# Optimization experiments

Hardware: AMD Instinct MI355X
Metric: run time of the kernel (lower is better)

The kernel has to match this reference:

```python
import jax, jax.numpy as jnp
import numpy as np

T, B, FEAT = 256, 512, 8
HID = 256
IN_DIM = 4  # QCNN output dim


def _linear_params(key, out_dim, in_dim, scale=0.1):
    kw, kb = jax.random.split(key)
    W = jax.random.normal(kw, (out_dim, in_dim), dtype=jnp.float32) * scale
    b = jax.random.normal(kb, (out_dim,), dtype=jnp.float32) * scale
    return W, b


def setup_inputs() -> dict:
    key = jax.random.key(0)
    ks = jax.random.split(key, 12)
    inputs = jax.random.normal(ks[0], (T, B, FEAT), dtype=jnp.float32)
    # QCNN feature extractor linears (torch Linear: W is [out, in])
    fm_w, fm_b = _linear_params(ks[1], 16, FEAT)
    c1_w, c1_b = _linear_params(ks[2], 16, 16)
    p1_w, p1_b = _linear_params(ks[3], 12, 16)
    c2_w, c2_b = _linear_params(ks[4], 8, 12)
    p2_w, p2_b = _linear_params(ks[5], 4, 8)
    c3_w, c3_b = _linear_params(ks[6], 4, 4)
    # LSTM gate linears: (IN_DIM + HID) -> HID
    f_w, f_b = _linear_params(ks[7], HID, IN_DIM + HID)
    i_w, i_b = _linear_params(ks[8], HID, IN_DIM + HID)
    u_w, u_b = _linear_params(ks[9], HID, IN_DIM + HID)
    o_w, o_b = _linear_params(ks[10], HID, IN_DIM + HID)
    # tagger head: HID -> 1
    head_w, head_b = _linear_params(ks[11], 1, HID)
    return dict(inputs=inputs, fm_w=fm_w, fm_b=fm_b, c1_w=c1_w, c1_b=c1_b,
                p1_w=p1_w, p1_b=p1_b, c2_w=c2_w, c2_b=c2_b, p2_w=p2_w, p2_b=p2_b,
                c3_w=c3_w, c3_b=c3_b, f_w=f_w, f_b=f_b, i_w=i_w, i_b=i_b,
                u_w=u_w, u_b=u_b, o_w=o_w, o_b=o_b, head_w=head_w, head_b=head_b)


def _lin(x, W, b):
    return x @ W.T + b


def reference(inputs, fm_w, fm_b, c1_w, c1_b, p1_w, p1_b, c2_w, c2_b,
              p2_w, p2_b, c3_w, c3_b, f_w, f_b, i_w, i_b, u_w, u_b,
              o_w, o_b, head_w, head_b):
    seq_len, batch, _ = inputs.shape
    # QCNN feature extractor has no cross-timestep dependency -> apply to all steps at once
    x = jnp.tanh(_lin(inputs, fm_w, fm_b))
    x = jnp.tanh(_lin(x, c1_w, c1_b))
    x = jnp.tanh(_lin(x, p1_w, p1_b))
    x = jnp.tanh(_lin(x, c2_w, c2_b))
    x = jnp.tanh(_lin(x, p2_w, p2_b))
    feats = jnp.tanh(_lin(x, c3_w, c3_b))  # [T, B, 4]

    h0 = jnp.zeros((batch, HID), dtype=inputs.dtype)
    c0 = jnp.zeros((batch, HID), dtype=inputs.dtype)

    def step(carry, xt):
        hx, cx = carry
        combined = jnp.concatenate([xt, hx], axis=1)  # [B, 4+HID]
        f = jax.nn.sigmoid(_lin(combined, f_w, f_b))
        i = jax.nn.sigmoid(_lin(combined, i_w, i_b))
        g = jnp.tanh(_lin(combined, u_w, u_b))
        o = jax.nn.sigmoid(_lin(combined, o_w, o_b))
        cx = f * cx + i * g
        hx = o * jnp.tanh(cx)
        return (hx, cx), hx

    (_, _), lstm_out = jax.lax.scan(step, (h0, c0), feats)  # [T, B, HID]
    out = _lin(lstm_out, head_w, head_b)  # [T, B, 1]
    return out
```

## Files before the change

### kernel.cpp

```cpp
#include <hip/hip_runtime.h>
#include <hip/hip_bf16.h>
#include <hip/hip_fp16.h>
#include <stdint.h>

#define T_STEPS 256
#define BATCH 512

typedef _Float16 f16x8 __attribute__((ext_vector_type(8)));
typedef _Float16 h2_t  __attribute__((ext_vector_type(2)));
typedef float    f32x4 __attribute__((ext_vector_type(4)));

__device__ __forceinline__ float fdot2(uint32_t w, uint32_t c, float acc) {
#if __has_builtin(__builtin_amdgcn_fdot2)
    h2_t a, b;
    __builtin_memcpy(&a, &w, 4);
    __builtin_memcpy(&b, &c, 4);
    return __builtin_amdgcn_fdot2(a, b, acc, false);
#else
    union { uint32_t u; _Float16 h[2]; } A, B;
    A.u = w; B.u = c;
    return acc + (float)A.h[0]*(float)B.h[0] + (float)A.h[1]*(float)B.h[1];
#endif
}

__device__ __forceinline__ float sigmoidf_(float x) {
    return 1.f / (1.f + __expf(-x));
}
__device__ __forceinline__ float tanhf_(float x) {
    float ax = fabsf(x);
    float e = __expf(-2.f * ax);
    float r = (1.f - e) / (1.f + e);
    return copysignf(r, x);
}

__device__ __forceinline__ float sel4(int d, float a, float b, float c, float e) {
    float lo = (d & 1) ? b : a;
    float hi = (d & 1) ? e : c;
    return (d & 2) ? hi : lo;
}

#define MFMA_AG(c, aa, bb) \
    asm volatile("v_mfma_f32_16x16x32_f16 %0, %1, %2, %0" : "+v"(c) : "v"(aa), "a"(bb))
#define MFMA_VG(c, aa, bb) \
    asm volatile("v_mfma_f32_16x16x32_f16 %0, %1, %2, %0" : "+v"(c) : "v"(aa), "v"(bb))

__global__ void concat_qw(const float* __restrict__ fm_w, const float* __restrict__ fm_b,
                          const float* __restrict__ c1_w, const float* __restrict__ c1_b,
                          const float* __restrict__ p1_w, const float* __restrict__ p1_b,
                          const float* __restrict__ c2_w, const float* __restrict__ c2_b,
                          const float* __restrict__ p2_w, const float* __restrict__ p2_b,
                          const float* __restrict__ c3_w, const float* __restrict__ c3_b,
                          float* __restrict__ qw) {
    for (int k = threadIdx.x; k < 780; k += 256) {
        float v;
        if      (k < 128) v = fm_w[k];
        else if (k < 144) v = fm_b[k-128];
        else if (k < 400) v = c1_w[k-144];
        else if (k < 416) v = c1_b[k-400];
        else if (k < 608) v = p1_w[k-416];
        else if (k < 620) v = p1_b[k-608];
        else if (k < 716) v = c2_w[k-620];
        else if (k < 724) v = c2_b[k-716];
        else if (k < 756) v = p2_w[k-724];
        else if (k < 760) v = p2_b[k-756];
        else if (k < 776) v = c3_w[k-760];
        else              v = c3_b[k-776];
        qw[k] = v;
    }
}

__global__ void pack_bfrag(const float* __restrict__ f_w, const float* __restrict__ i_w,
                           const float* __restrict__ u_w, const float* __restrict__ o_w,
                           uint4* __restrict__ bfragsG) {
    int idx = blockIdx.x * 256 + threadIdx.x;
    int l = idx & 63, q = (idx >> 6) & 7, n = idx >> 9;
    int col = n * 16 + (l & 15);
    int g = col >> 8, j = col & 255;
    const float* W = (g == 0) ? f_w : (g == 1) ? i_w : (g == 2) ? u_w : o_w;
    union { uint4 u; _Float16 h[8]; } P;
#pragma unroll
    for (int e = 0; e < 8; ++e) {
        int k = q * 32 + ((l >> 4) * 8) + e;
        P.h[e] = (_Float16)W[j * 260 + 4 + k];
    }
    bfragsG[idx] = P.u;
}

__global__ void pack_xw(const float* __restrict__ f_w, const float* __restrict__ i_w,
                        const float* __restrict__ u_w, const float* __restrict__ o_w,
                        _Float16* __restrict__ xwG) {
    int t = blockIdx.x * 256 + threadIdx.x;
    int g = t >> 10, k = (t >> 8) & 3, j = t & 255;
    const float* W = (g == 0) ? f_w : (g == 1) ? i_w : (g == 2) ? u_w : o_w;
    xwG[t] = (_Float16)W[j * 260 + k];
}

__global__ void qcnn_kernel(const float* __restrict__ in, const float* __restrict__ qw,
                            _Float16* __restrict__ feats) {
    int r = blockIdx.x * 256 + threadIdx.x;
    const float* x = in + (size_t)r * 8;
    float v0[8];
#pragma unroll
    for (int i = 0; i < 8; ++i) v0[i] = x[i];
    float v1[16];
#pragma unroll
    for (int o = 0; o < 16; ++o) {
        float s = qw[128 + o];
#pragma unroll
        for (int i = 0; i < 8; ++i) s += qw[o*8 + i] * v0[i];
        v1[o] = tanhf_(s);
    }
    float v2[16];
#pragma unroll
    for (int o = 0; o < 16; ++o) {
        float s = qw[400 + o];
#pragma unroll
        for (int i = 0; i < 16; ++i) s += qw[144 + o*16 + i] * v1[i];
        v2[o] = tanhf_(s);
    }
    float v3[12];
#pragma unroll
    for (int o = 0; o < 12; ++o) {
        float s = qw[608 + o];
#pragma unroll
        for (int i = 0; i < 16; ++i) s += qw[416 + o*16 + i] * v2[i];
        v3[o] = tanhf_(s);
    }
    float v4[8];
#pragma unroll
    for (int o = 0; o < 8; ++o) {
        float s = qw[716 + o];
#pragma unroll
        for (int i = 0; i < 12; ++i) s += qw[620 + o*12 + i] * v3[i];
        v4[o] = tanhf_(s);
    }
    float v5[4];
#pragma unroll
    for (int o = 0; o < 4; ++o) {
        float s = qw[756 + o];
#pragma unroll
        for (int i = 0; i < 8; ++i) s += qw[724 + o*8 + i] * v4[i];
        v5[o] = tanhf_(s);
    }
    union { uint32_t u[2]; _Float16 h[4]; } P;
#pragma unroll
    for (int o = 0; o < 4; ++o) {
        float s = qw[776 + o];
#pragma unroll
        for (int i = 0; i < 4; ++i) s += qw[760 + o*4 + i] * v5[i];
        P.h[o] = (_Float16)tanhf_(s);
    }
    *reinterpret_cast<uint2*>(feats + (size_t)r * 4) = make_uint2(P.u[0], P.u[1]);
}

__global__ __launch_bounds__(256, 1)
void lstm_kernel(const uint4* __restrict__ bfragsG, const _Float16* __restrict__ xwG,
                 const _Float16* __restrict__ feats,
                 const float* __restrict__ f_b, const float* __restrict__ i_b,
                 const float* __restrict__ u_b, const float* __restrict__ o_b,
                 const float* __restrict__ head_w, const float* __restrict__ head_bp,
                 float* __restrict__ out) {
    __shared__ uint4     blds67[2][64][64];
    __shared__ __align__(16) _Float16 comb[2][2][256];
    __shared__ float     redL[2][4][2];

    const int tid = threadIdx.x;
    const int w   = tid >> 6;
    const int l   = tid & 63;
    const int d_  = l >> 4;
    const int jl  = (w * 4 + d_) * 16 + (l & 15);
    const int s0  = blockIdx.x * 2;

    for (int idx = tid; idx < 8192; idx += 256) {
        int n = idx >> 7, qq = (idx >> 6) & 1, ll = idx & 63;
        blds67[qq][n][ll] = bfragsG[(n * 8 + 6 + qq) * 64 + ll];
    }
    reinterpret_cast<uint32_t*>(&comb[0][0][0])[tid] = 0u;

    f16x8 Br03[16][4];
#pragma unroll
    for (int m = 0; m < 16; ++m) {
        const int n = (m >> 2) * 16 + w * 4 + (m & 3);
#pragma unroll
        for (int q = 0; q < 4; ++q) {
            Br03[m][q] = *reinterpret_cast<const f16x8*>(bfragsG + (n * 8 + q) * 64 + l);
            asm volatile("" : "+a"(Br03[m][q]));
        }
    }
    f16x8 Br45[16][2];
#pragma unroll
    for (int m = 0; m < 16; ++m) {
        const int n = (m >> 2) * 16 + w * 4 + (m & 3);
#pragma unroll
        for (int q = 0; q < 2; ++q) {
            Br45[m][q] = *reinterpret_cast<const f16x8*>(bfragsG + (n * 8 + 4 + q) * 64 + l);
            asm volatile("" : "+v"(Br45[m][q]));
        }
    }

    float bias_[4] = { f_b[jl], i_b[jl], u_b[jl], o_b[jl] };
    uint32_t xwp0[4], xwp1[4];
#pragma unroll
    for (int g = 0; g < 4; ++g) {
        union { uint32_t u; _Float16 h[2]; } P;
        P.h[0] = xwG[g*1024 +       jl]; P.h[1] = xwG[g*1024 + 256 + jl];
        xwp0[g] = P.u;
        P.h[0] = xwG[g*1024 + 512 + jl]; P.h[1] = xwG[g*1024 + 768 + jl];
        xwp1[g] = P.u;
    }
    const float hwj = head_w[jl];
    const float hb  = head_bp[0];
    uint2 xr0 = *reinterpret_cast<const uint2*>(feats + ((size_t)0 * BATCH + s0    ) * 4);
    uint2 xr1 = *reinterpret_cast<const uint2*>(feats + ((size_t)0 * BATCH + s0 + 1) * 4);

    __syncthreads();

    float cs0 = 0.f, cs1 = 0.f;

#pragma unroll 1
    for (int t = 0; t < T_STEPS; ++t) {
        const int cur = t & 1;
        uint2 xn0 = xr0, xn1 = xr1;
        if (t + 1 < T_STEPS) {
            xn0 = *reinterpret_cast<const uint2*>(feats + ((size_t)(t+1) * BATCH + s0    ) * 4);
            xn1 = *reinterpret_cast<const uint2*>(feats + ((size_t)(t+1) * BATCH + s0 + 1) * 4);
        }

        const _Float16* ab = &comb[cur][l & 1][(l >> 4) * 8];
        f16x8 A_[8];
#pragma unroll
        for (int q = 0; q < 8; ++q)
            A_[q] = *reinterpret_cast<const f16x8*>(ab + q * 32);

        float gv0[4], gv1[4];

#pragma unroll
        for (int g = 0; g < 4; ++g) {
            f16x8 t6[4], t7[4];
#pragma unroll
            for (int d = 0; d < 4; ++d) {
                const int n = g * 16 + w * 4 + d;
                t6[d] = *reinterpret_cast<const f16x8*>(&blds67[0][n][l]);
                t7[d] = *reinterpret_cast<const f16x8*>(&blds67[1][n][l]);
            }

            f32x4 c0 = {0.f,0.f,0.f,0.f}, c1 = {0.f,0.f,0.f,0.f};
            f32x4 c2 = {0.f,0.f,0.f,0.f}, c3 = {0.f,0.f,0.f,0.f};
            asm volatile("s_nop 0" : "+v"(c0), "+v"(c1), "+v"(c2), "+v"(c3));

#pragma unroll
            for (int q = 0; q < 4; ++q) {
                MFMA_AG(c0, A_[q], Br03[4*g+0][q]); MFMA_AG(c1, A_[q], Br03[4*g+1][q]);
                MFMA_AG(c2, A_[q], Br03[4*g+2][q]); MFMA_AG(c3, A_[q], Br03[4*g+3][q]);
            }
#pragma unroll
            for (int q = 0; q < 2; ++q) {
                MFMA_VG(c0, A_[4+q], Br45[4*g+0][q]); MFMA_VG(c1, A_[4+q], Br45[4*g+1][q]);
                MFMA_VG(c2, A_[4+q], Br45[4*g+2][q]); MFMA_VG(c3, A_[4+q], Br45[4*g+3][q]);
            }
            c0 = __builtin_amdgcn_mfma_f32_16x16x32_f16(A_[6], t6[0], c0, 0, 0, 0);
            c1 = __builtin_amdgcn_mfma_f32_16x16x32_f16(A_[6], t6[1], c1, 0, 0, 0);
            c2 = __builtin_amdgcn_mfma_f32_16x16x32_f16(A_[6], t6[2], c2, 0, 0, 0);
            c3 = __builtin_amdgcn_mfma_f32_16x16x32_f16(A_[6], t6[3], c3, 0, 0, 0);
            c0 = __builtin_amdgcn_mfma_f32_16x16x32_f16(A_[7], t7[0], c0, 0, 0, 0);
            c1 = __builtin_amdgcn_mfma_f32_16x16x32_f16(A_[7], t7[1], c1, 0, 0, 0);
            c2 = __builtin_amdgcn_mfma_f32_16x16x32_f16(A_[7], t7[2], c2, 0, 0, 0);
            c3 = __builtin_amdgcn_mfma_f32_16x16x32_f16(A_[7], t7[3], c3, 0, 0, 0);

            gv0[g] = sel4(d_, c0[0], c1[0], c2[0], c3[0]);
            gv1[g] = sel4(d_, c0[1], c1[1], c2[1], c3[1]);
        }

        float pre0[4], pre1[4];
#pragma unroll
        for (int g = 0; g < 4; ++g) {
            pre0[g] = fdot2(xwp0[g], xr0.x, fdot2(xwp1[g], xr0.y, gv0[g] + bias_[g]));
            pre1[g] = fdot2(xwp0[g], xr1.x, fdot2(xwp1[g], xr1.y, gv1[g] + bias_[g]));
        }
        const float fg0 = sigmoidf_(pre0[0]), fg1 = sigmoidf_(pre1[0]);
        const float ig0 = sigmoidf_(pre0[1]), ig1 = sigmoidf_(pre1[1]);
        const float ug0 = tanhf_(pre0[2]),    ug1 = tanhf_(pre1[2]);
        const float og0 = sigmoidf_(pre0[3]), og1 = sigmoidf_(pre1[3]);
        cs0 = fg0 * cs0 + ig0 * ug0;
        cs1 = fg1 * cs1 + ig1 * ug1;
        const float h0 = og0 * tanhf_(cs0);
        const float h1 = og1 * tanhf_(cs1);

        comb[cur ^ 1][0][jl] = (_Float16)h0;
        comb[cur ^ 1][1][jl] = (_Float16)h1;

        xr0 = xn0; xr1 = xn1;
        __syncthreads();

        float p0 = h0 * hwj, p1 = h1 * hwj;
#pragma unroll
        for (int off = 32; off; off >>= 1) {
            p0 += __shfl_xor(p0, off);
            p1 += __shfl_xor(p1, off);
        }
        if (l == 0) { redL[cur][w][0] = p0; redL[cur][w][1] = p1; }

        if (tid < 2 && t > 0)
            out[(size_t)(t - 1) * BATCH + s0 + tid] =
                (redL[cur ^ 1][0][tid] + redL[cur ^ 1][1][tid]) +
                (redL[cur ^ 1][2][tid] + redL[cur ^ 1][3][tid]) + hb;
    }

    __syncthreads();
    if (tid < 2)
        out[(size_t)(T_STEPS - 1) * BATCH + s0 + tid] =
            (redL[(T_STEPS - 1) & 1][0][tid] + redL[(T_STEPS - 1) & 1][1][tid]) +
            (redL[(T_STEPS - 1) & 1][2][tid] + redL[(T_STEPS - 1) & 1][3][tid]) + hb;
}

extern "C" void kernel_launch(void* const* d_in, const int* in_sizes, int n_in,
                              void* d_out, int out_size, void* d_ws, size_t ws_size,
                              hipStream_t stream) {
    const float* inputs = (const float*)d_in[0];
    const float* fm_w = (const float*)d_in[1];  const float* fm_b = (const float*)d_in[2];
    const float* c1_w = (const float*)d_in[3];  const float* c1_b = (const float*)d_in[4];
    const float* p1_w = (const float*)d_in[5];  const float* p1_b = (const float*)d_in[6];
    const float* c2_w = (const float*)d_in[7];  const float* c2_b = (const float*)d_in[8];
    const float* p2_w = (const float*)d_in[9];  const float* p2_b = (const float*)d_in[10];
    const float* c3_w = (const float*)d_in[11]; const float* c3_b = (const float*)d_in[12];
    const float* f_w  = (const float*)d_in[13]; const float* f_b  = (const float*)d_in[14];
    const float* i_w  = (const float*)d_in[15]; const float* i_b  = (const float*)d_in[16];
    const float* u_w  = (const float*)d_in[17]; const float* u_b  = (const float*)d_in[18];
    const float* o_w  = (const float*)d_in[19]; const float* o_b  = (const float*)d_in[20];
    const float* head_w = (const float*)d_in[21];
    const float* head_b = (const float*)d_in[22];

    uint4*     bfragsG = (uint4*)d_ws;
    _Float16*  xwG     = (_Float16*)((char*)d_ws + 524288);
    _Float16*  feats   = (_Float16*)((char*)d_ws + 532480);
    float*     qw      = (float*)((char*)d_ws + 1581056);

    hipLaunchKernelGGL(concat_qw, dim3(1), dim3(256), 0, stream,
                       fm_w, fm_b, c1_w, c1_b, p1_w, p1_b, c2_w, c2_b,
                       p2_w, p2_b, c3_w, c3_b, qw);
    hipLaunchKernelGGL(pack_bfrag, dim3(128), dim3(256), 0, stream,
                       f_w, i_w, u_w, o_w, bfragsG);
    hipLaunchKernelGGL(pack_xw, dim3(16), dim3(256), 0, stream,
                       f_w, i_w, u_w, o_w, xwG);
    hipLaunchKernelGGL(qcnn_kernel, dim3(512), dim3(256), 0, stream,
                       inputs, qw, feats);
    hipLaunchKernelGGL(lstm_kernel, dim3(256), dim3(256), 0, stream,
                       bfragsG, xwG, feats,
                       f_b, i_b, u_b, o_b, head_w, head_b, (float*)d_out);
}
```

Before: 670.5 us.

## Split LSTM recurrence across eight waves per block with per-lane sample mapping

Doubles the LSTM block from 4 to 8 wavefronts so each wave computes only 2 of the 16-column tiles per gate instead of 4. Each lane now handles one sample and one hidden unit, which removes the duplicated dual-sample gate math and the 4-way select. Slices 4-5 of the weight fragments are now reloaded from global memory every step instead of being held in registers, and the feats prefetch for the next step is dropped. The goal is to shorten the per-step serial MFMA chain, at the cost of extra global loads per step and a barrier shared by more waves.

```diff
diff --git a/kernel.cpp b/kernel.cpp
--- a/kernel.cpp
+++ b/kernel.cpp
@@ -32,17 +32,6 @@
     float r = (1.f - e) / (1.f + e);
     return copysignf(r, x);
 }
-
-__device__ __forceinline__ float sel4(int d, float a, float b, float c, float e) {
-    float lo = (d & 1) ? b : a;
-    float hi = (d & 1) ? e : c;
-    return (d & 2) ? hi : lo;
-}
-
-#define MFMA_AG(c, aa, bb) \
-    asm volatile("v_mfma_f32_16x16x32_f16 %0, %1, %2, %0" : "+v"(c) : "v"(aa), "a"(bb))
-#define MFMA_VG(c, aa, bb) \
-    asm volatile("v_mfma_f32_16x16x32_f16 %0, %1, %2, %0" : "+v"(c) : "v"(aa), "v"(bb))
 
 __global__ void concat_qw(const float* __restrict__ fm_w, const float* __restrict__ fm_b,
                           const float* __restrict__ c1_w, const float* __restrict__ c1_b,
@@ -153,7 +142,7 @@
     *reinterpret_cast<uint2*>(feats + (size_t)r * 4) = make_uint2(P.u[0], P.u[1]);
 }
 
-__global__ __launch_bounds__(256, 1)
+__global__ __launch_bounds__(512, 2)
 void lstm_kernel(const uint4* __restrict__ bfragsG, const _Float16* __restrict__ xwG,
                  const _Float16* __restrict__ feats,
                  const float* __restrict__ f_b, const float* __restrict__ i_b,
@@ -162,39 +151,30 @@
                  float* __restrict__ out) {
     __shared__ uint4     blds67[2][64][64];
     __shared__ __align__(16) _Float16 comb[2][2][256];
-    __shared__ float     redL[2][4][2];
+    __shared__ float     redL[2][8][2];
 
     const int tid = threadIdx.x;
     const int w   = tid >> 6;
     const int l   = tid & 63;
-    const int d_  = l >> 4;
-    const int jl  = (w * 4 + d_) * 16 + (l & 15);
+    const int smp = l >> 5;
+    const int d_  = (l >> 4) & 1;
+    const int jl  = w * 32 + d_ * 16 + (l & 15);
     const int s0  = blockIdx.x * 2;
 
-    for (int idx = tid; idx < 8192; idx += 256) {
+    for (int idx = tid; idx < 8192; idx += 512) {
         int n = idx >> 7, qq = (idx >> 6) & 1, ll = idx & 63;
         blds67[qq][n][ll] = bfragsG[(n * 8 + 6 + qq) * 64 + ll];
     }
     reinterpret_cast<uint32_t*>(&comb[0][0][0])[tid] = 0u;
 
-    f16x8 Br03[16][4];
-#pragma unroll
-    for (int m = 0; m < 16; ++m) {
-        const int n = (m >> 2) * 16 + w * 4 + (m & 3);
+    f16x8 Br[8][4];
+#pragma unroll
+    for (int m = 0; m < 8; ++m) {
+        const int n = (m >> 1) * 16 + w * 2 + (m & 1);
 #pragma unroll
         for (int q = 0; q < 4; ++q) {
-            Br03[m][q] = *reinterpret_cast<const f16x8*>(bfragsG + (n * 8 + q) * 64 + l);
-            asm volatile("" : "+a"(Br03[m][q]));
-        }
-    }
-    f16x8 Br45[16][2];
-#pragma unroll
-    for (int m = 0; m < 16; ++m) {
-        const int n = (m >> 2) * 16 + w * 4 + (m & 3);
-#pragma unroll
-        for (int q = 0; q < 2; ++q) {
-            Br45[m][q] = *reinterpret_cast<const f16x8*>(bfragsG + (n * 8 + 4 + q) * 64 + l);
-            asm volatile("" : "+v"(Br45[m][q]));
+            Br[m][q] = *reinterpret_cast<const f16x8*>(bfragsG + (n * 8 + q) * 64 + l);
+            asm volatile("" : "+a"(Br[m][q]));
         }
     }
 
@@ -210,21 +190,16 @@
     }
     const float hwj = head_w[jl];
     const float hb  = head_bp[0];
-    uint2 xr0 = *reinterpret_cast<const uint2*>(feats + ((size_t)0 * BATCH + s0    ) * 4);
-    uint2 xr1 = *reinterpret_cast<const uint2*>(feats + ((size_t)0 * BATCH + s0 + 1) * 4);
 
     __syncthreads();
 
-    float cs0 = 0.f, cs1 = 0.f;
+    float cs = 0.f;
 
 #pragma unroll 1
     for (int t = 0; t < T_STEPS; ++t) {
         const int cur = t & 1;
-        uint2 xn0 = xr0, xn1 = xr1;
-        if (t + 1 < T_STEPS) {
-            xn0 = *reinterpret_cast<const uint2*>(feats + ((size_t)(t+1) * BATCH + s0    ) * 4);
-            xn1 = *reinterpret_cast<const uint2*>(feats + ((size_t)(t+1) * BATCH + s0 + 1) * 4);
-        }
+        const uint2 xr = *reinterpret_cast<const uint2*>(
+            feats + ((size_t)t * BATCH + s0 + smp) * 4);
 
         const _Float16* ab = &comb[cur][l & 1][(l >> 4) * 8];
         f16x8 A_[8];
@@ -232,85 +207,81 @@
         for (int q = 0; q < 8; ++q)
             A_[q] = *reinterpret_cast<const f16x8*>(ab + q * 32);
 
-        float gv0[4], gv1[4];
+        float pre[4];
 
 #pragma unroll
         for (int g = 0; g < 4; ++g) {
-            f16x8 t6[4], t7[4];
-#pragma unroll
-            for (int d = 0; d < 4; ++d) {
-                const int n = g * 16 + w * 4 + d;
-                t6[d] = *reinterpret_cast<const f16x8*>(&blds67[0][n][l]);
-                t7[d] = *reinterpret_cast<const f16x8*>(&blds67[1][n][l]);
+            const int n0 = g * 16 + w * 2;
+            const int n1 = n0 + 1;
+            f16x8 s4a = *reinterpret_cast<const f16x8*>(bfragsG + (n0 * 8 + 4) * 64 + l);
+            f16x8 s4b = *reinterpret_cast<const f16x8*>(bfragsG + (n1 * 8 + 4) * 64 + l);
+            f16x8 s5a = *reinterpret_cast<const f16x8*>(bfragsG + (n0 * 8 + 5) * 64 + l);
+            f16x8 s5b = *reinterpret_cast<const f16x8*>(bfragsG + (n1 * 8 + 5) * 64 + l);
+
+            f32x4 c0 = {0.f, 0.f, 0.f, 0.f};
+            f32x4 c1 = {0.f, 0.f, 0.f, 0.f};
+
+#pragma unroll
+            for (int q = 0; q < 4; ++q) {
+                c0 = __builtin_amdgcn_mfma_f32_16x16x32_f16(A_[q], Br[2*g    ][q], c0, 0, 0, 0);
+                c1 = __builtin_amdgcn_mfma_f32_16x16x32_f16(A_[q], Br[2*g + 1][q], c1, 0, 0, 0);
             }
-
-            f32x4 c0 = {0.f,0.f,0.f,0.f}, c1 = {0.f,0.f,0.f,0.f};
-            f32x4 c2 = {0.f,0.f,0.f,0.f}, c3 = {0.f,0.f,0.f,0.f};
-            asm volatile("s_nop 0" : "+v"(c0), "+v"(c1), "+v"(c2), "+v"(c3));
-
-#pragma unroll
-            for (int q = 0; q < 4; ++q) {
-                MFMA_AG(c0, A_[q], Br03[4*g+0][q]); MFMA_AG(c1, A_[q], Br03[4*g+1][q]);
-                MFMA_AG(c2, A_[q], Br03[4*g+2][q]); MFMA_AG(c3, A_[q], Br03[4*g+3][q]);
-            }
-#pragma unroll
-            for (int q = 0; q < 2; ++q) {
-                MFMA_VG(c0, A_[4+q], Br45[4*g+0][q]); MFMA_VG(c1, A_[4+q], Br45[4*g+1][q]);
-                MFMA_VG(c2, A_[4+q], Br45[4*g+2][q]); MFMA_VG(c3, A_[4+q], Br45[4*g+3][q]);
-            }
-            c0 = __builtin_amdgcn_mfma_f32_16x16x32_f16(A_[6], t6[0], c0, 0, 0, 0);
-            c1 = __builtin_amdgcn_mfma_f32_16x16x32_f16(A_[6], t6[1], c1, 0, 0, 0);
-            c2 = __builtin_amdgcn_mfma_f32_16x16x32_f16(A_[6], t6[2], c2, 0, 0, 0);
-            c3 = __builtin_amdgcn_mfma_f32_16x16x32_f16(A_[6], t6[3], c3, 0, 0, 0);
-            c0 = __builtin_amdgcn_mfma_f32_16x16x32_f16(A_[7], t7[0], c0, 0, 0, 0);
-            c1 = __builtin_amdgcn_mfma_f32_16x16x32_f16(A_[7], t7[1], c1, 0, 0, 0);
-            c2 = __builtin_amdgcn_mfma_f32_16x16x32_f16(A_[7], t7[2], c2, 0, 0, 0);
-            c3 = __builtin_amdgcn_mfma_f32_16x16x32_f16(A_[7], t7[3], c3, 0, 0, 0);
-
-            gv0[g] = sel4(d_, c0[0], c1[0], c2[0], c3[0]);
-            gv1[g] = sel4(d_, c0[1], c1[1], c2[1], c3[1]);
+            c0 = __builtin_amdgcn_mfma_f32_16x16x32_f16(A_[4], s4a, c0, 0, 0, 0);
+            c1 = __builtin_amdgcn_mfma_f32_16x16x32_f16(A_[4], s4b, c1, 0, 0, 0);
+            c0 = __builtin_amdgcn_mfma_f32_16x16x32_f16(A_[5], s5a, c0, 0, 0, 0);
+            c1 = __builtin_amdgcn_mfma_f32_16x16x32_f16(A_[5], s5b, c1, 0, 0, 0);
+            f16x8 t6a = *reinterpret_cast<const f16x8*>(&blds67[0][n0][l]);
+            f16x8 t6b = *reinterpret_cast<const f16x8*>(&blds67[0][n1][l]);
+            c0 = __builtin_amdgcn_mfma_f32_16x16x32_f16(A_[6], t6a, c0, 0, 0, 0);
+            c1 = __builtin_amdgcn_mfma_f32_16x16x32_f16(A_[6], t6b, c1, 0, 0, 0);
+            f16x8 t7a = *reinterpret_cast<const f16x8*>(&blds67[1][n0][l]);
+            f16x8 t7b = *reinterpret_cast<const f16x8*>(&blds67[1][n1][l]);
+            c0 = __builtin_amdgcn_mfma_f32_16x16x32_f16(A_[7], t7a, c0, 0, 0, 0);
+            c1 = __builtin_amdgcn_mfma_f32_16x16x32_f16(A_[7], t7b, c1, 0, 0, 0);
+
+            const float va = smp ? c0[1] : c0[0];
+            const float vb = smp ? c1[1] : c1[0];
+            pre[g] = (d_ ? vb : va) + bias_[g];
         }
 
-        float pre0[4], pre1[4];
-#pragma unroll
-        for (int g = 0; g < 4; ++g) {
-            pre0[g] = fdot2(xwp0[g], xr0.x, fdot2(xwp1[g], xr0.y, gv0[g] + bias_[g]));
-            pre1[g] = fdot2(xwp0[g], xr1.x, fdot2(xwp1[g], xr1.y, gv1[g] + bias_[g]));
+        float p0 = fdot2(xwp0[0], xr.x, fdot2(xwp1[0], xr.y, pre[0]));
+        float p1 = fdot2(xwp0[1], xr.x, fdot2(xwp1[1], xr.y, pre[1]));
+        float p2 = fdot2(xwp0[2], xr.x, fdot2(xwp1[2], xr.y, pre[2]));
+        float p3 = fdot2(xwp0[3], xr.x, fdot2(xwp1[3], xr.y, pre[3]));
+        const float fg = sigmoidf_(p0);
+        const float ig = sigmoidf_(p1);
+        const float ug = tanhf_(p2);
+        const float og = sigmoidf_(p3);
+        cs = fg * cs + ig * ug;
+        const float h = og * tanhf_(cs);
+
+        comb[cur ^ 1][smp][jl] = (_Float16)h;
+
+        __syncthreads();
+
+        float p = h * hwj;
+        p += __shfl_xor(p, 1);
+        p += __shfl_xor(p, 2);
+        p += __shfl_xor(p, 4);
+        p += __shfl_xor(p, 8);
+        p += __shfl_xor(p, 16);
+        if ((l & 31) == 0) redL[cur][w][smp] = p;
+
+        if (tid < 2 && t > 0) {
+            float acc = hb;
+#pragma unroll
+            for (int ww = 0; ww < 8; ++ww) acc += redL[cur ^ 1][ww][tid];
+            out[(size_t)(t - 1) * BATCH + s0 + tid] = acc;
         }
-        const float fg0 = sigmoidf_(pre0[0]), fg1 = sigmoidf_(pre1[0]);
-        const float ig0 = sigmoidf_(pre0[1]), ig1 = sigmoidf_(pre1[1]);
-        const float ug0 = tanhf_(pre0[2]),    ug1 = tanhf_(pre1[2]);
-        const float og0 = sigmoidf_(pre0[3]), og1 = sigmoidf_(pre1[3]);
-        cs0 = fg0 * cs0 + ig0 * ug0;
-        cs1 = fg1 * cs1 + ig1 * ug1;
-        const float h0 = og0 * tanhf_(cs0);
-        const float h1 = og1 * tanhf_(cs1);
-
-        comb[cur ^ 1][0][jl] = (_Float16)h0;
-        comb[cur ^ 1][1][jl] = (_Float16)h1;
-
-        xr0 = xn0; xr1 = xn1;
-        __syncthreads();
-
-        float p0 = h0 * hwj, p1 = h1 * hwj;
-#pragma unroll
-        for (int off = 32; off; off >>= 1) {
-            p0 += __shfl_xor(p0, off);
-            p1 += __shfl_xor(p1, off);
-        }
-        if (l == 0) { redL[cur][w][0] = p0; redL[cur][w][1] = p1; }
-
-        if (tid < 2 && t > 0)
-            out[(size_t)(t - 1) * BATCH + s0 + tid] =
-                (redL[cur ^ 1][0][tid] + redL[cur ^ 1][1][tid]) +
-                (redL[cur ^ 1][2][tid] + redL[cur ^ 1][3][tid]) + hb;
     }
 
     __syncthreads();
-    if (tid < 2)
-        out[(size_t)(T_STEPS - 1) * BATCH + s0 + tid] =
-            (redL[(T_STEPS - 1) & 1][0][tid] + redL[(T_STEPS - 1) & 1][1][tid]) +
-            (redL[(T_STEPS - 1) & 1][2][tid] + redL[(T_STEPS - 1) & 1][3][tid]) + hb;
+    if (tid < 2) {
+        float acc = hb;
+#pragma unroll
+        for (int ww = 0; ww < 8; ++ww) acc += redL[(T_STEPS - 1) & 1][ww][tid];
+        out[(size_t)(T_STEPS - 1) * BATCH + s0 + tid] = acc;
+    }
 }
 
 extern "C" void kernel_launch(void* const* d_in, const int* in_sizes, int n_in,
@@ -344,7 +315,7 @@
                        f_w, i_w, u_w, o_w, xwG);
     hipLaunchKernelGGL(qcnn_kernel, dim3(512), dim3(256), 0, stream,
                        inputs, qw, feats);
-    hipLaunchKernelGGL(lstm_kernel, dim3(256), dim3(256), 0, stream,
+    hipLaunchKernelGGL(lstm_kernel, dim3(256), dim3(512), 0, stream,
                        bfragsG, xwG, feats,
                        f_b, i_b, u_b, o_b, head_w, head_b, (float*)d_out);
 }
```

Result: slower. 684.6 us (+2.1%).
